# Kernel tuning notes

Measured on AMD Instinct MI355X. Metric: run time of the kernel, lower is better.

Reference implementation:

```python
import jax, jax.numpy as jnp
import numpy as np

N, M = 49, 4  # fixed by module: H=W=7, sh=sw=2

def _ln(x, g, b, eps=1e-5):
    mu = jnp.mean(x, axis=-1, keepdims=True)
    var = jnp.var(x, axis=-1, keepdims=True)
    return (x - mu) / jnp.sqrt(var + eps) * g + b

def setup_inputs() -> dict:
    key = jax.random.key(0)
    ks = jax.random.split(key, 12)
    B, C = 256, 768
    Cf = 4 * C
    s = 0.02
    return {
        "x":      jax.random.normal(ks[0], (B, N, M, C), jnp.float32),
        "ln1_g":  jnp.ones((C,), jnp.float32),
        "ln1_b":  jnp.zeros((C,), jnp.float32),
        "w_qkv":  jax.random.normal(ks[1], (3 * C, C), jnp.float32) * s,
        "w_proj": jax.random.normal(ks[2], (C, C), jnp.float32) * s,
        "b_proj": jnp.zeros((C,), jnp.float32),
        "mix":    jax.random.normal(ks[3], (1, N, M, 1, 2), jnp.float32),
        "ln2_g":  jnp.ones((C,), jnp.float32),
        "ln2_b":  jnp.zeros((C,), jnp.float32),
        "w_fc1":  jax.random.normal(ks[4], (Cf, C), jnp.float32) * s,
        "b_fc1":  jnp.zeros((Cf,), jnp.float32),
        "w_fc2":  jax.random.normal(ks[5], (C, Cf), jnp.float32) * s,
        "b_fc2":  jnp.zeros((C,), jnp.float32),
    }

def reference(x, ln1_g, ln1_b, w_qkv, w_proj, b_proj, mix, ln2_g, ln2_b,
              w_fc1, b_fc1, w_fc2, b_fc2):
    B, n, m, C = x.shape  # n=49, m=4
    h = 12
    c = C // h
    scale = c ** -0.5

    x_ = _ln(x, ln1_g, ln1_b)
    qkv = jnp.einsum('bnmc,dc->bnmd', x_, w_qkv)            # [B,N,M,3C]
    qkv = qkv.reshape(B, n, m, 3, h, c)
    q, k, v = qkv[..., 0, :, :], qkv[..., 1, :, :], qkv[..., 2, :, :]  # [B,N,M,h,c]

    # attention over M axis (seq len 4), per (b, n)
    qm = q.transpose(0, 1, 3, 2, 4)  # [B,N,h,M,c]
    km = k.transpose(0, 1, 3, 2, 4)
    vm = v.transpose(0, 1, 3, 2, 4)
    am = jax.nn.softmax(jnp.einsum('bnhmc,bnhpc->bnhmp', qm, km) * scale, axis=-1)
    x_m = jnp.einsum('bnhmp,bnhpc->bnhmc', am, vm)
    x_m = x_m.transpose(0, 1, 3, 2, 4).reshape(B, n, m, C)

    # attention over N axis (seq len 49), per (b, m)
    qn = q.transpose(0, 2, 3, 1, 4)  # [B,M,h,N,c]
    kn = k.transpose(0, 2, 3, 1, 4)
    vn = v.transpose(0, 2, 3, 1, 4)
    an = jax.nn.softmax(jnp.einsum('bmhnc,bmhpc->bmhnp', qn, kn) * scale, axis=-1)
    x_n = jnp.einsum('bmhnp,bmhpc->bmhnc', an, vn)
    x_n = x_n.transpose(0, 3, 1, 2, 4).reshape(B, n, m, C)

    # learned softmax mix: stack order is [x_n, x_m]
    w = jax.nn.softmax(mix, axis=-1)  # [1,N,M,1,2]
    x_ = x_n * w[..., 0] + x_m * w[..., 1]

    x_ = jnp.einsum('bnmc,dc->bnmd', x_, w_proj) + b_proj
    x = x + x_

    y = _ln(x, ln2_g, ln2_b)
    y = jax.nn.gelu(jnp.einsum('bnmc,fc->bnmf', y, w_fc1) + b_fc1, approximate=False)
    y = jnp.einsum('bnmf,cf->bnmc', y, w_fc2) + b_fc2
    return x + y
```

## Files before the change

### kernel.cpp

```cpp
#include <hip/hip_runtime.h>
#include <hip/hip_bf16.h>
#include <math.h>


typedef __attribute__((ext_vector_type(8))) short short8;
typedef __attribute__((ext_vector_type(4))) float floatx4;

__device__ __forceinline__ float bf2f(unsigned short s) {
    union { float f; unsigned u; } z; z.u = ((unsigned)s) << 16; return z.f;
}
__device__ __forceinline__ unsigned short f2bf(float f) {
    union { float f; unsigned u; } z; z.f = f;
    unsigned r = z.u + 0x7fffu + ((z.u >> 16) & 1u);
    return (unsigned short)(r >> 16);
}

__global__ __launch_bounds__(256) void cvt4_kernel(const float4* __restrict__ s0,
                                                   const float4* __restrict__ s1,
                                                   const float4* __restrict__ s2,
                                                   const float4* __restrict__ s3,
                                                   ushort4* __restrict__ d0,
                                                   ushort4* __restrict__ d1,
                                                   ushort4* __restrict__ d2,
                                                   ushort4* __restrict__ d3) {
    int i = blockIdx.x * 256 + threadIdx.x;
    const float4* s; ushort4* d; int off;
    if (i < 442368)       { s = s0; d = d0; off = i; }
    else if (i < 589824)  { s = s1; d = d1; off = i - 442368; }
    else if (i < 1179648) { s = s2; d = d2; off = i - 589824; }
    else                  { s = s3; d = d3; off = i - 1179648; }
    const float4 v = s[off];
    ushort4 o;
    o.x = f2bf(v.x); o.y = f2bf(v.y); o.z = f2bf(v.z); o.w = f2bf(v.w);
    d[off] = o;
}

__global__ __launch_bounds__(192) void ln_kernel(const float* __restrict__ x,
                                                 const float* __restrict__ g,
                                                 const float* __restrict__ b,
                                                 unsigned short* __restrict__ out) {
    const int tid = threadIdx.x;
    const size_t base = (size_t)blockIdx.x * 768 + tid * 4;
    const float4 v = *(const float4*)(x + base);
    float s  = v.x + v.y + v.z + v.w;
    float s2 = v.x * v.x + v.y * v.y + v.z * v.z + v.w * v.w;
#pragma unroll
    for (int off = 32; off; off >>= 1) { s += __shfl_xor(s, off); s2 += __shfl_xor(s2, off); }
    __shared__ float red[6];
    const int wave = tid >> 6, lane = tid & 63;
    if (lane == 0) { red[wave] = s; red[wave + 3] = s2; }
    __syncthreads();
    s  = red[0] + red[1] + red[2];
    s2 = red[3] + red[4] + red[5];
    const float mu  = s * (1.0f / 768.0f);
    const float inv = rsqrtf(s2 * (1.0f / 768.0f) - mu * mu + 1e-5f);
    const float4 gv = *(const float4*)(g + tid * 4);
    const float4 bv = *(const float4*)(b + tid * 4);
    ushort4 o;
    o.x = f2bf((v.x - mu) * inv * gv.x + bv.x);
    o.y = f2bf((v.y - mu) * inv * gv.y + bv.y);
    o.z = f2bf((v.z - mu) * inv * gv.z + bv.z);
    o.w = f2bf((v.w - mu) * inv * gv.w + bv.w);
    *(ushort4*)(out + base) = o;
}

template <int EPI>
__global__ __launch_bounds__(256, 2)
void gemm_bt(const unsigned short* __restrict__ A,
             const unsigned short* __restrict__ B,
             const float* __restrict__ bias,
             const float* __restrict__ resid,
             unsigned short* __restrict__ outB,
             float* __restrict__ outF,
             int M, int N, int K) {
    __shared__ __attribute__((aligned(16))) unsigned short As[128 * 32];
    __shared__ __attribute__((aligned(16))) unsigned short Bs[128 * 32];
    const int tid  = threadIdx.x;
    const int lane = tid & 63, wave = tid >> 6;
    const int wr = wave >> 1, wc = wave & 1;
    const int nwg = gridDim.x;
    const int q8 = nwg >> 3, r8 = nwg & 7;
    const int xcd = blockIdx.x & 7, loc = blockIdx.x >> 3;
    const int wgid = (xcd < r8 ? xcd * (q8 + 1) : r8 * (q8 + 1) + (xcd - r8) * q8) + loc;
    const int tileN = N >> 7;
    const int bx = wgid % tileN;
    const int by = wgid / tileN;
    const size_t row0 = (size_t)by << 7;
    const int col0 = bx << 7;

    floatx4 acc[4][4];
#pragma unroll
    for (int i = 0; i < 4; ++i)
#pragma unroll
        for (int j = 0; j < 4; ++j) acc[i][j] = (floatx4)(0.0f);

    const int c8  = (lane & 3) << 3;
    const int rA0 = (wave << 5) + (lane >> 2);
    const int ldsOff0 = (wave * 2) * 512 + lane * 8;

    for (int k0 = 0; k0 < K; k0 += 32) {
        short8 ta[2], tb[2];
#pragma unroll
        for (int j = 0; j < 2; ++j) {
            const size_t rA = row0 + rA0 + j * 16;
            const size_t ra = (rA < (size_t)M) ? rA : (size_t)(M - 1);
            ta[j] = *(const short8*)(A + ra * K + k0 + c8);
            tb[j] = *(const short8*)(B + (size_t)(col0 + rA0 + j * 16) * K + k0 + c8);
        }
        __syncthreads();
#pragma unroll
        for (int j = 0; j < 2; ++j) {
            *(short8*)(As + ldsOff0 + j * 512) = ta[j];
            *(short8*)(Bs + ldsOff0 + j * 512) = tb[j];
        }
        __syncthreads();
        short8 af[4], bfv[4];
        const int lr = lane & 15, lk = (lane >> 4) << 3;
#pragma unroll
        for (int mi = 0; mi < 4; ++mi)
            af[mi] = *(const short8*)(As + ((wr << 6) + (mi << 4) + lr) * 32 + lk);
#pragma unroll
        for (int ni = 0; ni < 4; ++ni)
            bfv[ni] = *(const short8*)(Bs + ((wc << 6) + (ni << 4) + lr) * 32 + lk);
#pragma unroll
        for (int mi = 0; mi < 4; ++mi)
#pragma unroll
            for (int ni = 0; ni < 4; ++ni)
                acc[mi][ni] = __builtin_amdgcn_mfma_f32_16x16x32_bf16(af[mi], bfv[ni], acc[mi][ni], 0, 0, 0);
    }

    const int er = (lane >> 4) << 2;
    const int ec = lane & 15;
#pragma unroll
    for (int mi = 0; mi < 4; ++mi)
#pragma unroll
        for (int ni = 0; ni < 4; ++ni)
#pragma unroll
            for (int r = 0; r < 4; ++r) {
                const size_t row = row0 + (wr << 6) + (mi << 4) + er + r;
                if (row >= (size_t)M) continue;
                const int col = col0 + (wc << 6) + (ni << 4) + ec;
                const size_t o = row * N + col;
                float v = acc[mi][ni][r];
                if constexpr (EPI == 0) {
                    outB[o] = f2bf(v);
                } else if constexpr (EPI == 1) {
                    outF[o] = v + bias[col] + resid[o];
                } else {
                    float hh = v + bias[col];
                    outB[o] = f2bf(0.5f * hh * (1.0f + erff(hh * 0.70710678118654752f)));
                }
            }
}

__global__ __launch_bounds__(256) void attn_n_kernel(const unsigned short* __restrict__ qkv,
                                                     unsigned short* __restrict__ xn) {
    __shared__ __attribute__((aligned(16))) unsigned short lds[4 * 9216];
    const int tid = threadIdx.x, lane = tid & 63, wave = tid >> 6;
    const int hg = blockIdx.x % 3;
    const int bm = blockIdx.x / 3;
    const int m = bm & 3, b = bm >> 2;
    const int h = hg * 4 + wave;
    const int lr = lane & 15, hi = lane >> 4;
    unsigned short* Ps  = lds + wave * 9216;
    unsigned short* vsT = Ps + 4608;

    for (int c = lane; c < 392; c += 64) {
        const int p = c >> 3, cc0 = (c & 7) << 3;
        const size_t vb = ((size_t)((b * 49 + p) * 4 + m)) * 2304 + 1536 + h * 64 + cc0;
        const short8 v = *(const short8*)(qkv + vb);
#pragma unroll
        for (int j = 0; j < 8; ++j) {
            const int cc = cc0 + j;
            vsT[cc * 72 + (p ^ ((cc >> 3) << 3))] = (unsigned short)v[j];
        }
    }
#pragma unroll
    for (int it = 0; it < 15; ++it) {
        const int cc = lane, p = 49 + it;
        vsT[cc * 72 + (p ^ ((cc >> 3) << 3))] = 0;
    }

    short8 qf[4][2], kf[4][2];
#pragma unroll
    for (int mi = 0; mi < 4; ++mi) {
        int q = mi * 16 + lr; q = (q > 48) ? 48 : q;
        const size_t qb = ((size_t)((b * 49 + q) * 4 + m)) * 2304 + h * 64;
#pragma unroll
        for (int ks = 0; ks < 2; ++ks) {
            qf[mi][ks] = *(const short8*)(qkv + qb + ks * 32 + hi * 8);
            kf[mi][ks] = *(const short8*)(qkv + qb + 768 + ks * 32 + hi * 8);
        }
    }
    floatx4 acc[4][4];
#pragma unroll
    for (int i = 0; i < 4; ++i)
#pragma unroll
        for (int j = 0; j < 4; ++j) acc[i][j] = (floatx4)(0.0f);
#pragma unroll
    for (int ks = 0; ks < 2; ++ks)
#pragma unroll
        for (int mi = 0; mi < 4; ++mi)
#pragma unroll
            for (int ni = 0; ni < 4; ++ni)
                acc[mi][ni] = __builtin_amdgcn_mfma_f32_16x16x32_bf16(qf[mi][ks], kf[ni][ks], acc[mi][ni], 0, 0, 0);

#pragma unroll
    for (int mi = 0; mi < 4; ++mi)
#pragma unroll
        for (int ni = 0; ni < 4; ++ni) {
            const int col = ni * 16 + lr;
#pragma unroll
            for (int r = 0; r < 4; ++r)
                acc[mi][ni][r] = (col < 49) ? acc[mi][ni][r] * 0.125f : -1e30f;
        }
#pragma unroll
    for (int mi = 0; mi < 4; ++mi) {
#pragma unroll
        for (int r = 0; r < 4; ++r) {
            float mx = fmaxf(fmaxf(acc[mi][0][r], acc[mi][1][r]), fmaxf(acc[mi][2][r], acc[mi][3][r]));
#pragma unroll
            for (int off = 8; off; off >>= 1) mx = fmaxf(mx, __shfl_xor(mx, off));
            float e0 = expf(acc[mi][0][r] - mx), e1 = expf(acc[mi][1][r] - mx);
            float e2 = expf(acc[mi][2][r] - mx), e3 = expf(acc[mi][3][r] - mx);
            float sum = e0 + e1 + e2 + e3;
#pragma unroll
            for (int off = 8; off; off >>= 1) sum += __shfl_xor(sum, off);
            const float inv = 1.0f / sum;
            const int row = mi * 16 + hi * 4 + r;
            Ps[row * 72 + 0  + lr] = f2bf(e0 * inv);
            Ps[row * 72 + 16 + lr] = f2bf(e1 * inv);
            Ps[row * 72 + 32 + lr] = f2bf(e2 * inv);
            Ps[row * 72 + 48 + lr] = f2bf(e3 * inv);
        }
    }

    floatx4 oac[4][4];
#pragma unroll
    for (int i = 0; i < 4; ++i)
#pragma unroll
        for (int j = 0; j < 4; ++j) oac[i][j] = (floatx4)(0.0f);
#pragma unroll
    for (int ks = 0; ks < 2; ++ks) {
        short8 pf[4], vf[4];
        const int p0 = ks * 32 + hi * 8;
#pragma unroll
        for (int mi = 0; mi < 4; ++mi)
            pf[mi] = *(const short8*)(Ps + (mi * 16 + lr) * 72 + p0);
#pragma unroll
        for (int ni = 0; ni < 4; ++ni) {
            const int cc = ni * 16 + lr;
            vf[ni] = *(const short8*)(vsT + cc * 72 + (p0 ^ ((cc >> 3) << 3)));
        }
#pragma unroll
        for (int mi = 0; mi < 4; ++mi)
#pragma unroll
            for (int ni = 0; ni < 4; ++ni)
                oac[mi][ni] = __builtin_amdgcn_mfma_f32_16x16x32_bf16(pf[mi], vf[ni], oac[mi][ni], 0, 0, 0);
    }

#pragma unroll
    for (int mi = 0; mi < 4; ++mi)
#pragma unroll
        for (int r = 0; r < 4; ++r) {
            const int row = mi * 16 + hi * 4 + r;
            if (row >= 49) continue;
            const size_t ob = ((size_t)((b * 49 + row) * 4 + m)) * 768 + h * 64;
#pragma unroll
            for (int ni = 0; ni < 4; ++ni)
                xn[ob + ni * 16 + lr] = f2bf(oac[mi][ni][r]);
        }
}

__global__ __launch_bounds__(256) void attn_m_kernel(const unsigned short* __restrict__ qkv,
                                                     const float* __restrict__ mixp,
                                                     unsigned short* __restrict__ xn) {
    __shared__ __attribute__((aligned(16))) float qs[4 * 12 * 68], ks[4 * 12 * 68], vs[4 * 12 * 68];
    __shared__ float as[192];
    const int tid = threadIdx.x;
    const size_t tbase = (size_t)blockIdx.x * 4;
    const int n = blockIdx.x % 49;

    for (int c = tid; c < 384; c += 256) {
        const int mq = c / 96;
        const int rem = c - mq * 96;
        const int hh = rem >> 3, cc0 = (rem & 7) << 3;
        const size_t base = (tbase + mq) * 2304 + hh * 64 + cc0;
        const short8 qv = *(const short8*)(qkv + base);
        const short8 kv = *(const short8*)(qkv + base + 768);
        const short8 vv = *(const short8*)(qkv + base + 1536);
        const int slot = (mq * 12 + hh) * 68 + cc0;
#pragma unroll
        for (int j = 0; j < 4; ++j) {
            float4 fq, fk, fv;
            (void)fq; (void)fk; (void)fv;
        }
        float4 f;
        f.x = bf2f((unsigned short)qv[0]); f.y = bf2f((unsigned short)qv[1]);
        f.z = bf2f((unsigned short)qv[2]); f.w = bf2f((unsigned short)qv[3]);
        *(float4*)(qs + slot) = f;
        f.x = bf2f((unsigned short)qv[4]); f.y = bf2f((unsigned short)qv[5]);
        f.z = bf2f((unsigned short)qv[6]); f.w = bf2f((unsigned short)qv[7]);
        *(float4*)(qs + slot + 4) = f;
        f.x = bf2f((unsigned short)kv[0]); f.y = bf2f((unsigned short)kv[1]);
        f.z = bf2f((unsigned short)kv[2]); f.w = bf2f((unsigned short)kv[3]);
        *(float4*)(ks + slot) = f;
        f.x = bf2f((unsigned short)kv[4]); f.y = bf2f((unsigned short)kv[5]);
        f.z = bf2f((unsigned short)kv[6]); f.w = bf2f((unsigned short)kv[7]);
        *(float4*)(ks + slot + 4) = f;
        f.x = bf2f((unsigned short)vv[0]); f.y = bf2f((unsigned short)vv[1]);
        f.z = bf2f((unsigned short)vv[2]); f.w = bf2f((unsigned short)vv[3]);
        *(float4*)(vs + slot) = f;
        f.x = bf2f((unsigned short)vv[4]); f.y = bf2f((unsigned short)vv[5]);
        f.z = bf2f((unsigned short)vv[6]); f.w = bf2f((unsigned short)vv[7]);
        *(float4*)(vs + slot + 4) = f;
    }
    __syncthreads();

    if (tid < 192) {
        const int hh = tid >> 4, m = (tid >> 2) & 3, p = tid & 3;
        const float* q = qs + (m * 12 + hh) * 68;
        const float* k = ks + (p * 12 + hh) * 68;
        float s = 0.f;
#pragma unroll
        for (int cc = 0; cc < 64; ++cc) s += q[cc] * k[cc];
        as[tid] = s * 0.125f;
    }
    __syncthreads();
    if (tid < 48) {
        float* a = as + tid * 4;
        float mx = fmaxf(fmaxf(a[0], a[1]), fmaxf(a[2], a[3]));
        float e0 = expf(a[0] - mx), e1 = expf(a[1] - mx), e2 = expf(a[2] - mx), e3 = expf(a[3] - mx);
        float inv = 1.f / (e0 + e1 + e2 + e3);
        a[0] = e0 * inv; a[1] = e1 * inv; a[2] = e2 * inv; a[3] = e3 * inv;
    }
    __syncthreads();

    float w0[4], w1[4];
#pragma unroll
    for (int m = 0; m < 4; ++m) {
        const float m0 = mixp[(n * 4 + m) * 2], m1 = mixp[(n * 4 + m) * 2 + 1];
        const float mx = fmaxf(m0, m1);
        const float e0 = expf(m0 - mx), e1 = expf(m1 - mx);
        w0[m] = e0 / (e0 + e1);
        w1[m] = 1.0f - w0[m];
    }

    for (int o = tid; o < 3072; o += 256) {
        const int cc = o & 63, m = (o >> 6) & 3, hh = o >> 8;
        const float* a = as + hh * 16 + m * 4;
        float r = a[0] * vs[(0 * 12 + hh) * 68 + cc] + a[1] * vs[(1 * 12 + hh) * 68 + cc]
                + a[2] * vs[(2 * 12 + hh) * 68 + cc] + a[3] * vs[(3 * 12 + hh) * 68 + cc];
        const size_t oidx = (tbase + m) * 768 + hh * 64 + cc;
        const float vn = bf2f(xn[oidx]);
        xn[oidx] = f2bf(vn * w0[m] + r * w1[m]);
    }
}

extern "C" void kernel_launch(void* const* d_in, const int* in_sizes, int n_in,
                              void* d_out, int out_size, void* d_ws, size_t ws_size,
                              hipStream_t stream) {
    const float* x      = (const float*)d_in[0];
    const float* ln1_g  = (const float*)d_in[1];
    const float* ln1_b  = (const float*)d_in[2];
    const float* w_qkv  = (const float*)d_in[3];
    const float* w_proj = (const float*)d_in[4];
    const float* b_proj = (const float*)d_in[5];
    const float* mixp   = (const float*)d_in[6];
    const float* ln2_g  = (const float*)d_in[7];
    const float* ln2_b  = (const float*)d_in[8];
    const float* w_fc1  = (const float*)d_in[9];
    const float* b_fc1  = (const float*)d_in[10];
    const float* w_fc2  = (const float*)d_in[11];
    const float* b_fc2  = (const float*)d_in[12];
    float* out = (float*)d_out;

    char* ws = (char*)d_ws;
    unsigned short* wqkv_bf  = (unsigned short*)(ws);
    unsigned short* wproj_bf = (unsigned short*)(ws + 3538944);
    unsigned short* wfc1_bf  = (unsigned short*)(ws + 4718592);
    unsigned short* wfc2_bf  = (unsigned short*)(ws + 9437184);

    int CB = 64;
    while (CB > 1 && 14155776ull + (size_t)CB * 196 * 7680 > ws_size) CB >>= 1;
    const int nch = 256 / CB;
    const int TC = CB * 196;
    const int rowT = (TC + 127) >> 7;
    unsigned short* xbuf  = (unsigned short*)(ws + 14155776);
    unsigned short* qkv_c = (unsigned short*)(ws + 14155776 + (size_t)TC * 1536);

    dim3 blk(256);
    cvt4_kernel<<<6912, blk, 0, stream>>>((const float4*)w_qkv, (const float4*)w_proj,
                                          (const float4*)w_fc1, (const float4*)w_fc2,
                                          (ushort4*)wqkv_bf, (ushort4*)wproj_bf,
                                          (ushort4*)wfc1_bf, (ushort4*)wfc2_bf);

    for (int i = 0; i < nch; ++i) {
        const size_t r0 = (size_t)i * TC;
        const float* xc = x + r0 * 768;
        float* x2c = out + r0 * 768;

        ln_kernel<<<TC, dim3(192), 0, stream>>>(xc, ln1_g, ln1_b, xbuf);
        gemm_bt<0><<<rowT * 18, blk, 0, stream>>>(xbuf, wqkv_bf, nullptr, nullptr, qkv_c, nullptr, TC, 2304, 768);
        attn_n_kernel<<<CB * 12, blk, 0, stream>>>(qkv_c, xbuf);
        attn_m_kernel<<<CB * 49, blk, 0, stream>>>(qkv_c, mixp, xbuf);
        gemm_bt<1><<<rowT * 6, blk, 0, stream>>>(xbuf, wproj_bf, b_proj, xc, nullptr, x2c, TC, 768, 768);
        ln_kernel<<<TC, dim3(192), 0, stream>>>(x2c, ln2_g, ln2_b, xbuf);
        gemm_bt<2><<<rowT * 24, blk, 0, stream>>>(xbuf, wfc1_bf, b_fc1, nullptr, qkv_c, nullptr, TC, 3072, 768);
        gemm_bt<1><<<rowT * 6, blk, 0, stream>>>(qkv_c, wfc2_bf, b_fc2, x2c, nullptr, x2c, TC, 768, 3072);
    }
}
```

Before: 1.927 ms.

## Prefetch next K-tile into registers and XOR-swizzle LDS layout in GEMM

The GEMM main loop now issues the global loads for the next 32-wide K slice into registers before running the MFMAs on the current slice, so memory latency overlaps with compute. The LDS tile layout also changes from a linear per-lane layout to a row-major layout with an XOR swizzle on the 8-element column chunk, meant to avoid bank conflicts on fragment reads. The cost is extra registers for the prefetched fragments, which may lower occupancy. A dead placeholder loop in the attention kernel is also removed.

After: 1.922 ms. Within noise of the previous version (-0.2%).

```diff
diff --git a/kernel.cpp b/kernel.cpp
--- a/kernel.cpp
+++ b/kernel.cpp
@@ -96,37 +96,51 @@
 
     const int c8  = (lane & 3) << 3;
     const int rA0 = (wave << 5) + (lane >> 2);
-    const int ldsOff0 = (wave * 2) * 512 + lane * 8;
+    const int wslot = (((lane & 3) ^ ((lane >> 3) & 3)) << 3);
+    const int lr = lane & 15;
+    const int rs = (((lane >> 4) ^ ((lr >> 1) & 3)) << 3);
+
+    short8 ta[2], tb[2], na[2], nb[2];
+#pragma unroll
+    for (int j = 0; j < 2; ++j) {
+        const size_t rA = row0 + rA0 + j * 16;
+        const size_t ra = (rA < (size_t)M) ? rA : (size_t)(M - 1);
+        ta[j] = *(const short8*)(A + ra * K + c8);
+        tb[j] = *(const short8*)(B + (size_t)(col0 + rA0 + j * 16) * K + c8);
+    }
 
     for (int k0 = 0; k0 < K; k0 += 32) {
-        short8 ta[2], tb[2];
+        __syncthreads();
 #pragma unroll
         for (int j = 0; j < 2; ++j) {
-            const size_t rA = row0 + rA0 + j * 16;
-            const size_t ra = (rA < (size_t)M) ? rA : (size_t)(M - 1);
-            ta[j] = *(const short8*)(A + ra * K + k0 + c8);
-            tb[j] = *(const short8*)(B + (size_t)(col0 + rA0 + j * 16) * K + k0 + c8);
+            *(short8*)(As + (rA0 + j * 16) * 32 + wslot) = ta[j];
+            *(short8*)(Bs + (rA0 + j * 16) * 32 + wslot) = tb[j];
         }
         __syncthreads();
-#pragma unroll
-        for (int j = 0; j < 2; ++j) {
-            *(short8*)(As + ldsOff0 + j * 512) = ta[j];
-            *(short8*)(Bs + ldsOff0 + j * 512) = tb[j];
-        }
-        __syncthreads();
+        const int kn = k0 + 32;
+        if (kn < K) {
+#pragma unroll
+            for (int j = 0; j < 2; ++j) {
+                const size_t rA = row0 + rA0 + j * 16;
+                const size_t ra = (rA < (size_t)M) ? rA : (size_t)(M - 1);
+                na[j] = *(const short8*)(A + ra * K + kn + c8);
+                nb[j] = *(const short8*)(B + (size_t)(col0 + rA0 + j * 16) * K + kn + c8);
+            }
+        }
         short8 af[4], bfv[4];
-        const int lr = lane & 15, lk = (lane >> 4) << 3;
 #pragma unroll
         for (int mi = 0; mi < 4; ++mi)
-            af[mi] = *(const short8*)(As + ((wr << 6) + (mi << 4) + lr) * 32 + lk);
+            af[mi] = *(const short8*)(As + ((wr << 6) + (mi << 4) + lr) * 32 + rs);
 #pragma unroll
         for (int ni = 0; ni < 4; ++ni)
-            bfv[ni] = *(const short8*)(Bs + ((wc << 6) + (ni << 4) + lr) * 32 + lk);
+            bfv[ni] = *(const short8*)(Bs + ((wc << 6) + (ni << 4) + lr) * 32 + rs);
 #pragma unroll
         for (int mi = 0; mi < 4; ++mi)
 #pragma unroll
             for (int ni = 0; ni < 4; ++ni)
                 acc[mi][ni] = __builtin_amdgcn_mfma_f32_16x16x32_bf16(af[mi], bfv[ni], acc[mi][ni], 0, 0, 0);
+#pragma unroll
+        for (int j = 0; j < 2; ++j) { ta[j] = na[j]; tb[j] = nb[j]; }
     }
 
     const int er = (lane >> 4) << 2;
@@ -290,11 +304,6 @@
         const short8 kv = *(const short8*)(qkv + base + 768);
         const short8 vv = *(const short8*)(qkv + base + 1536);
         const int slot = (mq * 12 + hh) * 68 + cc0;
-#pragma unroll
-        for (int j = 0; j < 4; ++j) {
-            float4 fq, fk, fv;
-            (void)fq; (void)fk; (void)fv;
-        }
         float4 f;
         f.x = bf2f((unsigned short)qv[0]); f.y = bf2f((unsigned short)qv[1]);
         f.z = bf2f((unsigned short)qv[2]); f.w = bf2f((unsigned short)qv[3]);
```
